# Optimization experiments

Measured on AMD Instinct MI355X. Metric: run time of the kernel, lower is better.

Reference implementation:

```python
import jax, jax.numpy as jnp
import numpy as np


def setup_inputs() -> dict:
    key = jax.random.key(0)
    k1, k2 = jax.random.split(key)
    B, S, D, K = 16, 2048, 256, 512
    features = jax.random.normal(k1, (B, S, D), dtype=jnp.float32)
    Ck = jax.random.normal(k2, (1, K, D), dtype=jnp.float32)
    return {"features": features, "Ck": Ck}


def reference(features, Ck):
    # features: (B, S, D); Ck: (1, K, D)
    # Squared euclidean distance to each of K centers: (B, S, K)
    # Computed as ||f||^2 + ||c||^2 - 2 f.c to avoid the (B*S, K, D) diff tensor.
    C = Ck[0]                                   # (K, D)
    f_sq = jnp.sum(features * features, axis=-1, keepdims=True)   # (B, S, 1)
    c_sq = jnp.sum(C * C, axis=-1)                                # (K,)
    cross = jnp.einsum("bsd,kd->bsk", features, C)               # (B, S, K)
    return f_sq + c_sq[None, None, :] - 2.0 * cross
```

## Files before the change

kernel.cpp:

```cpp
#include <hip/hip_runtime.h>

typedef __attribute__((ext_vector_type(8))) short bf16x8;
typedef __attribute__((ext_vector_type(4))) float f32x4;

#define BM 128
#define BN 128

__device__ inline unsigned short f2bf(float f) {
  unsigned int u = __builtin_bit_cast(unsigned int, f);
  u += 0x7fffu + ((u >> 16) & 1u);
  return (unsigned short)(u >> 16);
}

__device__ inline void gload16(const void* g, void* l) {
  __builtin_amdgcn_global_load_lds(
      (const __attribute__((address_space(1))) void*)g,
      (__attribute__((address_space(3))) void*)l, 16, 0, 0);
}

__global__ void prep_c(const float* __restrict__ C, unsigned short* __restrict__ Cbf,
                       float* __restrict__ csq, int K) {
  const int w = threadIdx.x >> 6, lane = threadIdx.x & 63;
  const int row = blockIdx.x * 4 + w;
  if (row >= K) return;
  const float4 v = *reinterpret_cast<const float4*>(&C[(size_t)row * 256 + lane * 4]);
  ushort4 b;
  b.x = f2bf(v.x); b.y = f2bf(v.y); b.z = f2bf(v.z); b.w = f2bf(v.w);
  const int boff = (lane * 8) ^ ((row & 7) << 4);
  *reinterpret_cast<ushort4*>((char*)Cbf + (size_t)row * 512 + boff) = b;
  float sq = v.x * v.x + v.y * v.y + v.z * v.z + v.w * v.w;
#pragma unroll
  for (int o = 32; o; o >>= 1) sq += __shfl_xor(sq, o);
  if (lane == 0) csq[row] = sq;
}

__global__ __launch_bounds__(256, 3) void dist_fused(
    const float* __restrict__ F, const unsigned short* __restrict__ Cbf,
    const float* __restrict__ csq, float* __restrict__ out, int M, int N) {
  __shared__ __align__(16) char Asb[BM * 256];
  __shared__ __align__(16) char Bsb[BN * 128];
  __shared__ float fsq_s[BM];

  const int t = threadIdx.x;
  const int w = t >> 6, lane = t & 63;
  const int wr = w >> 1, wc = w & 1;
  const int rl = lane & 15, kh = lane >> 4;
  const int amask = (rl & 7) << 4;

  const int nwg = gridDim.x;
  const int cpx = nwg >> 3;
  const int work = (blockIdx.x & 7) * cpx + (blockIdx.x >> 3);
  const int ntiles = N / BN;
  const int n0 = (work % ntiles) * BN;
  const int m0 = (work / ntiles) * BM;

  float cs[4];
#pragma unroll
  for (int ni = 0; ni < 4; ni++) cs[ni] = csq[n0 + wc * 64 + ni * 16 + rl];

  f32x4 acc[4][4];
#pragma unroll
  for (int i = 0; i < 4; i++)
#pragma unroll
    for (int j = 0; j < 4; j++) acc[i][j] = (f32x4){0.f, 0.f, 0.f, 0.f};
  float rsq[4] = {0.f, 0.f, 0.f, 0.f};

  const int a_r16 = t >> 4;
  const int a_cb = ((t & 15) * 16) ^ ((a_r16 & 7) << 4);
  const int b_r32 = t >> 3;
  const int b_cb = (t & 7) * 16;

  for (int kt = 0; kt < 4; ++kt) {
#pragma unroll
    for (int j = 0; j < 8; ++j)
      gload16((const char*)F + (size_t)(m0 + j * 16 + a_r16) * 1024 + kt * 256 + a_cb,
              Asb + j * 4096 + w * 1024);
#pragma unroll
    for (int j = 0; j < 4; ++j)
      gload16((const char*)Cbf + (size_t)(n0 + j * 32 + b_r32) * 512 + kt * 128 + b_cb,
              Bsb + j * 4096 + w * 1024);
    __syncthreads();

#pragma unroll
    for (int kk = 0; kk < 2; ++kk) {
      bf16x8 bfr[4];
#pragma unroll
      for (int ni = 0; ni < 4; ni++)
        bfr[ni] = *reinterpret_cast<const bf16x8*>(
            Bsb + (wc * 64 + ni * 16 + rl) * 128 + ((kk * 64 + kh * 16) ^ amask));
#pragma unroll
      for (int mi = 0; mi < 4; mi++) {
        const char* arow = Asb + (wr * 64 + mi * 16 + rl) * 256;
        const int c0 = (kk * 128 + kh * 32) ^ amask;
        const int c1 = (kk * 128 + kh * 32 + 16) ^ amask;
        const f32x4 a0 = *reinterpret_cast<const f32x4*>(arow + c0);
        const f32x4 a1 = *reinterpret_cast<const f32x4*>(arow + c1);
        rsq[mi] += a0[0] * a0[0] + a0[1] * a0[1] + a0[2] * a0[2] + a0[3] * a0[3] +
                   a1[0] * a1[0] + a1[1] * a1[1] + a1[2] * a1[2] + a1[3] * a1[3];
        bf16x8 af;
        af[0] = (short)f2bf(a0[0]); af[1] = (short)f2bf(a0[1]);
        af[2] = (short)f2bf(a0[2]); af[3] = (short)f2bf(a0[3]);
        af[4] = (short)f2bf(a1[0]); af[5] = (short)f2bf(a1[1]);
        af[6] = (short)f2bf(a1[2]); af[7] = (short)f2bf(a1[3]);
#pragma unroll
        for (int ni = 0; ni < 4; ni++)
          acc[mi][ni] = __builtin_amdgcn_mfma_f32_16x16x32_bf16(
              af, bfr[ni], acc[mi][ni], 0, 0, 0);
      }
    }
    __syncthreads();
  }

#pragma unroll
  for (int mi = 0; mi < 4; mi++) {
    float v = rsq[mi];
    v += __shfl_xor(v, 16);
    v += __shfl_xor(v, 32);
    if (wc == 0 && lane < 16) fsq_s[wr * 64 + mi * 16 + lane] = v;
  }
  __syncthreads();

#pragma unroll
  for (int mi = 0; mi < 4; mi++) {
    const int rloc = wr * 64 + mi * 16 + kh * 4;
    float fr[4];
#pragma unroll
    for (int r = 0; r < 4; r++) fr[r] = fsq_s[rloc + r];
#pragma unroll
    for (int ni = 0; ni < 4; ni++) {
      const int cloc = wc * 64 + ni * 16 + rl;
#pragma unroll
      for (int r = 0; r < 4; r++)
        out[(size_t)(m0 + rloc + r) * N + n0 + cloc] =
            fr[r] + cs[ni] - 2.0f * acc[mi][ni][r];
    }
  }
}

extern "C" void kernel_launch(void* const* d_in, const int* in_sizes, int n_in,
                              void* d_out, int out_size, void* d_ws, size_t ws_size,
                              hipStream_t stream) {
  const float* F = (const float*)d_in[0];
  const float* C = (const float*)d_in[1];
  float* out = (float*)d_out;
  const int D = 256;
  const int M = in_sizes[0] / D;
  const int N = in_sizes[1] / D;

  unsigned short* Cbf = (unsigned short*)d_ws;
  float* csq = (float*)(Cbf + (size_t)N * D);

  hipLaunchKernelGGL(prep_c, dim3(N / 4), dim3(256), 0, stream, C, Cbf, csq, N);
  const int nwg = (M / BM) * (N / BN);
  hipLaunchKernelGGL(dist_fused, dim3(nwg), dim3(256), 0, stream,
                     F, Cbf, csq, out, M, N);
}
```

Measured before the change: 37.16 us.

## Double-buffer K-loop with smaller K tiles, swap MFMA operands for vectorized stores

```diff
diff --git a/kernel.cpp b/kernel.cpp
--- a/kernel.cpp
+++ b/kernel.cpp
@@ -5,6 +5,8 @@
 
 #define BM 128
 #define BN 128
+#define BKA 32
+#define NKT 8
 
 __device__ inline unsigned short f2bf(float f) {
   unsigned int u = __builtin_bit_cast(unsigned int, f);
@@ -26,7 +28,7 @@
   const float4 v = *reinterpret_cast<const float4*>(&C[(size_t)row * 256 + lane * 4]);
   ushort4 b;
   b.x = f2bf(v.x); b.y = f2bf(v.y); b.z = f2bf(v.z); b.w = f2bf(v.w);
-  const int boff = (lane * 8) ^ ((row & 7) << 4);
+  const int boff = (lane * 8) ^ ((row & 3) << 4);
   *reinterpret_cast<ushort4*>((char*)Cbf + (size_t)row * 512 + boff) = b;
   float sq = v.x * v.x + v.y * v.y + v.z * v.z + v.w * v.w;
 #pragma unroll
@@ -37,15 +39,15 @@
 __global__ __launch_bounds__(256, 3) void dist_fused(
     const float* __restrict__ F, const unsigned short* __restrict__ Cbf,
     const float* __restrict__ csq, float* __restrict__ out, int M, int N) {
-  __shared__ __align__(16) char Asb[BM * 256];
-  __shared__ __align__(16) char Bsb[BN * 128];
-  __shared__ float fsq_s[BM];
+  __shared__ __align__(16) char As[2][BM * 128];
+  __shared__ __align__(16) char Bs[2][BN * 64];
 
   const int t = threadIdx.x;
   const int w = t >> 6, lane = t & 63;
   const int wr = w >> 1, wc = w & 1;
   const int rl = lane & 15, kh = lane >> 4;
-  const int amask = (rl & 7) << 4;
+  const int amaskA = (rl & 7) << 4;
+  const int amaskB = (rl & 3) << 4;
 
   const int nwg = gridDim.x;
   const int cpx = nwg >> 3;
@@ -54,9 +56,31 @@
   const int n0 = (work % ntiles) * BN;
   const int m0 = (work / ntiles) * BM;
 
-  float cs[4];
+  const int a_row = t >> 3;
+  const int a_cb = ((t & 7) * 16) ^ ((a_row & 7) << 4);
+  const char* Asrc = (const char*)F + (size_t)(m0 + a_row) * 1024 + a_cb;
+  const int b_row = t >> 2;
+  const int b_cb = (t & 3) * 16;
+  const char* Bsrc = (const char*)Cbf + (size_t)(n0 + b_row) * 512 + b_cb;
+
+#define STAGE(KT, BUF)                                                        \
+  {                                                                           \
+    _Pragma("unroll")                                                         \
+    for (int j = 0; j < 4; ++j)                                               \
+      gload16(Asrc + (size_t)j * 32768 + (KT) * 128,                          \
+              (char*)As[BUF] + j * 4096 + w * 1024);                          \
+    _Pragma("unroll")                                                         \
+    for (int j = 0; j < 2; ++j)                                               \
+      gload16(Bsrc + (size_t)j * 32768 + (KT) * 64,                           \
+              (char*)Bs[BUF] + j * 4096 + w * 1024);                          \
+  }
+
+  STAGE(0, 0)
+
+  float4 cs4[4];
 #pragma unroll
-  for (int ni = 0; ni < 4; ni++) cs[ni] = csq[n0 + wc * 64 + ni * 16 + rl];
+  for (int ni = 0; ni < 4; ni++)
+    cs4[ni] = *reinterpret_cast<const float4*>(&csq[n0 + wc * 64 + ni * 16 + kh * 4]);
 
   f32x4 acc[4][4];
 #pragma unroll
@@ -65,74 +89,66 @@
     for (int j = 0; j < 4; j++) acc[i][j] = (f32x4){0.f, 0.f, 0.f, 0.f};
   float rsq[4] = {0.f, 0.f, 0.f, 0.f};
 
-  const int a_r16 = t >> 4;
-  const int a_cb = ((t & 15) * 16) ^ ((a_r16 & 7) << 4);
-  const int b_r32 = t >> 3;
-  const int b_cb = (t & 7) * 16;
+#pragma unroll
+  for (int kt = 0; kt < NKT; ++kt) {
+    const int cur = kt & 1;
+    if (kt < NKT - 1) {
+      STAGE(kt + 1, cur ^ 1)
+      asm volatile("s_waitcnt vmcnt(6)" ::: "memory");
+    } else {
+      asm volatile("s_waitcnt vmcnt(0)" ::: "memory");
+    }
+    __builtin_amdgcn_s_barrier();
+    asm volatile("" ::: "memory");
 
-  for (int kt = 0; kt < 4; ++kt) {
+    bf16x8 bfr[4];
 #pragma unroll
-    for (int j = 0; j < 8; ++j)
-      gload16((const char*)F + (size_t)(m0 + j * 16 + a_r16) * 1024 + kt * 256 + a_cb,
-              Asb + j * 4096 + w * 1024);
-#pragma unroll
-    for (int j = 0; j < 4; ++j)
-      gload16((const char*)Cbf + (size_t)(n0 + j * 32 + b_r32) * 512 + kt * 128 + b_cb,
-              Bsb + j * 4096 + w * 1024);
-    __syncthreads();
+    for (int ni = 0; ni < 4; ni++)
+      bfr[ni] = *reinterpret_cast<const bf16x8*>(
+          (const char*)Bs[cur] + (wc * 64 + ni * 16 + rl) * 64 + ((kh * 16) ^ amaskB));
 
 #pragma unroll
-    for (int kk = 0; kk < 2; ++kk) {
-      bf16x8 bfr[4];
+    for (int mi = 0; mi < 4; mi++) {
+      const char* arow = (const char*)As[cur] + (wr * 64 + mi * 16 + rl) * 128;
+      const f32x4 a0 = *reinterpret_cast<const f32x4*>(arow + ((kh * 32) ^ amaskA));
+      const f32x4 a1 = *reinterpret_cast<const f32x4*>(arow + ((kh * 32 + 16) ^ amaskA));
+      rsq[mi] += a0[0] * a0[0] + a0[1] * a0[1] + a0[2] * a0[2] + a0[3] * a0[3] +
+                 a1[0] * a1[0] + a1[1] * a1[1] + a1[2] * a1[2] + a1[3] * a1[3];
+      bf16x8 af;
+      af[0] = (short)f2bf(a0[0]); af[1] = (short)f2bf(a0[1]);
+      af[2] = (short)f2bf(a0[2]); af[3] = (short)f2bf(a0[3]);
+      af[4] = (short)f2bf(a1[0]); af[5] = (short)f2bf(a1[1]);
+      af[6] = (short)f2bf(a1[2]); af[7] = (short)f2bf(a1[3]);
 #pragma unroll
       for (int ni = 0; ni < 4; ni++)
-        bfr[ni] = *reinterpret_cast<const bf16x8*>(
-            Bsb + (wc * 64 + ni * 16 + rl) * 128 + ((kk * 64 + kh * 16) ^ amask));
-#pragma unroll
-      for (int mi = 0; mi < 4; mi++) {
-        const char* arow = Asb + (wr * 64 + mi * 16 + rl) * 256;
-        const int c0 = (kk * 128 + kh * 32) ^ amask;
-        const int c1 = (kk * 128 + kh * 32 + 16) ^ amask;
-        const f32x4 a0 = *reinterpret_cast<const f32x4*>(arow + c0);
-        const f32x4 a1 = *reinterpret_cast<const f32x4*>(arow + c1);
-        rsq[mi] += a0[0] * a0[0] + a0[1] * a0[1] + a0[2] * a0[2] + a0[3] * a0[3] +
-                   a1[0] * a1[0] + a1[1] * a1[1] + a1[2] * a1[2] + a1[3] * a1[3];
-        bf16x8 af;
-        af[0] = (short)f2bf(a0[0]); af[1] = (short)f2bf(a0[1]);
-        af[2] = (short)f2bf(a0[2]); af[3] = (short)f2bf(a0[3]);
-        af[4] = (short)f2bf(a1[0]); af[5] = (short)f2bf(a1[1]);
-        af[6] = (short)f2bf(a1[2]); af[7] = (short)f2bf(a1[3]);
-#pragma unroll
-        for (int ni = 0; ni < 4; ni++)
-          acc[mi][ni] = __builtin_amdgcn_mfma_f32_16x16x32_bf16(
-              af, bfr[ni], acc[mi][ni], 0, 0, 0);
-      }
+        acc[mi][ni] = __builtin_amdgcn_mfma_f32_16x16x32_bf16(
+            bfr[ni], af, acc[mi][ni], 0, 0, 0);
     }
-    __syncthreads();
+    __builtin_amdgcn_s_barrier();
+    asm volatile("" ::: "memory");
   }
 
+  float fv[4];
 #pragma unroll
   for (int mi = 0; mi < 4; mi++) {
     float v = rsq[mi];
     v += __shfl_xor(v, 16);
     v += __shfl_xor(v, 32);
-    if (wc == 0 && lane < 16) fsq_s[wr * 64 + mi * 16 + lane] = v;
+    fv[mi] = v;
   }
-  __syncthreads();
 
 #pragma unroll
   for (int mi = 0; mi < 4; mi++) {
-    const int rloc = wr * 64 + mi * 16 + kh * 4;
-    float fr[4];
-#pragma unroll
-    for (int r = 0; r < 4; r++) fr[r] = fsq_s[rloc + r];
+    const int m = m0 + wr * 64 + mi * 16 + rl;
 #pragma unroll
     for (int ni = 0; ni < 4; ni++) {
-      const int cloc = wc * 64 + ni * 16 + rl;
-#pragma unroll
-      for (int r = 0; r < 4; r++)
-        out[(size_t)(m0 + rloc + r) * N + n0 + cloc] =
-            fr[r] + cs[ni] - 2.0f * acc[mi][ni][r];
+      const int n = n0 + wc * 64 + ni * 16 + kh * 4;
+      float4 v;
+      v.x = fv[mi] + cs4[ni].x - 2.0f * acc[mi][ni][0];
+      v.y = fv[mi] + cs4[ni].y - 2.0f * acc[mi][ni][1];
+      v.z = fv[mi] + cs4[ni].z - 2.0f * acc[mi][ni][2];
+      v.w = fv[mi] + cs4[ni].w - 2.0f * acc[mi][ni][3];
+      *reinterpret_cast<float4*>(&out[(size_t)m * N + n]) = v;
     }
   }
 }
```

Result: slower. 124.3 us (+234.4%).
